# Performance work log

Hardware: AMD Instinct MI355X
Metric: run time of the kernel (lower is better)

The kernel has to match this reference:

```python
import jax, jax.numpy as jnp
import numpy as np

B, H, W = 32, 512, 384
V, F = 6890, 13776


def setup_inputs() -> dict:
    key = jax.random.key(0)
    ks = jax.random.split(key, 8)
    scale = jnp.array([W, H, 1.0], dtype=jnp.float32)
    verts_1 = jax.random.uniform(ks[0], (B, V, 3), dtype=jnp.float32) * scale
    verts_2 = jax.random.uniform(ks[1], (B, V, 3), dtype=jnp.float32) * scale
    # face index per pixel; -1 = background (uint32 0xFFFFFFFF sentinel in original)
    vis_1 = (jax.random.randint(ks[2], (B, H, W), 0, F + 1) - 1).astype(jnp.int32)
    vis_2 = (jax.random.randint(ks[3], (B, H, W), 0, F + 1) - 1).astype(jnp.int32)
    face = jax.random.randint(ks[4], (F, 3), 0, V).astype(jnp.int32)
    vis_sym_mask_1 = (jax.random.uniform(ks[5], (B, H, W)) < 0.5).astype(jnp.float32)
    sym = jax.random.randint(ks[6], (V,), 0, V)
    symmetric_table = jnp.concatenate([sym, jnp.array([-1])]).astype(jnp.int32)
    return {"verts_1": verts_1, "vis_1": vis_1, "verts_2": verts_2, "vis_2": vis_2,
            "face": face, "vis_sym_mask_1": vis_sym_mask_1, "symmetric_table": symmetric_table}


def _pix_grid(h, w):
    # (x, y) pixel coordinates, shape [h, w, 2]
    x = jnp.arange(w, dtype=jnp.float32)
    y = jnp.arange(h, dtype=jnp.float32)
    return jnp.stack(jnp.meshgrid(x, y, indexing="xy"), axis=-1)


def reference(verts_1, vis_1, verts_2, vis_2, face, vis_sym_mask_1, symmetric_table):
    v1 = verts_1[:, :, :2]  # [B,V,2]
    v2 = verts_2[:, :, :2]
    bg = vis_1 < 0
    fc = jnp.where(bg, 0, vis_1)  # safe face id per pixel

    # --- vis_2_onehot: which faces are visible in image 2 ---
    valid2 = vis_2 >= 0
    idx2 = jnp.where(valid2, vis_2, 0)
    bidx = jnp.arange(B)[:, None, None]
    vf2 = jnp.zeros((B, F), jnp.int32).at[bidx, idx2].add(valid2.astype(jnp.int32)) > 0

    # --- cal_corr: barycentric correspondence per pixel ---
    tri = face[fc]  # [B,H,W,3] vertex ids of the face under each pixel
    gather = jax.vmap(lambda verts, t: verts[t])  # per-batch fancy gather
    p1 = gather(v1, tri)  # [B,H,W,3,2] face verts in img1
    p = _pix_grid(H, W)  # [H,W,2]
    a, b_, c = p1[..., 0, :], p1[..., 1, :], p1[..., 2, :]
    e0, e1, e2 = b_ - a, c - a, p - a
    d00 = (e0 * e0).sum(-1); d01 = (e0 * e1).sum(-1); d11 = (e1 * e1).sum(-1)
    d20 = (e2 * e0).sum(-1); d21 = (e2 * e1).sum(-1)
    denom = d00 * d11 - d01 * d01
    denom = jnp.where(jnp.abs(denom) < 1e-12, 1.0, denom)
    wv = (d11 * d20 - d01 * d21) / denom
    ww = (d00 * d21 - d01 * d20) / denom
    bary = jnp.stack([1.0 - wv - ww, wv, ww], axis=-1)  # [B,H,W,3]

    vis2f = vf2[bidx, fc]  # face visible in img2?
    sym_tri = symmetric_table[tri]  # symmetric vertex ids (-1 = none)
    sym_ok = jnp.all(sym_tri >= 0, axis=-1) & (vis_sym_mask_1 > 0)
    use_sym = (~vis2f) & sym_ok & (~bg)
    tri2 = jnp.where(use_sym[..., None], jnp.where(sym_tri >= 0, sym_tri, 0), tri)
    p2 = gather(v2, tri2)  # [B,H,W,3,2] face verts in img2
    corr = jnp.einsum("bhwk,bhwkc->bhwc", bary, p2)  # [B,H,W,2] (u,v)

    has_corr = (~bg) & (vis2f | use_sym)
    corr_mask = jnp.where(bg, 2.0, jnp.where(has_corr, 0.0, 1.0)).astype(jnp.float32)
    corr = jnp.where(has_corr[..., None], corr, 0.0)

    # custom kernel outputs are detached in the original
    corr = jax.lax.stop_gradient(corr)
    corr_mask = jax.lax.stop_gradient(corr_mask)

    # --- pad to square ---
    pad = (H - W) // 2
    corr = corr + jnp.array([pad, 0], dtype=corr.dtype)
    corr = jnp.pad(corr, ((0, 0), (0, 0), (pad, pad), (0, 0)))
    corr_mask = jnp.pad(corr_mask[..., None], ((0, 0), (0, 0), (pad, pad), (0, 0)),
                        constant_values=2.0)  # [B,H,W+2p,1]
    Hp, Wp = H, W + 2 * pad

    # --- corr_to_flow (HWC) then fix_flow: grid = base + (corr - base), normalized ---
    base = _pix_grid(Hp, Wp)  # [Hp,Wp,2]
    flow = corr - base
    grid = base + flow
    gx = 2.0 * grid[..., 0] / max(Wp - 1, 1) - 1.0
    gy = 2.0 * grid[..., 1] / max(Hp - 1, 1) - 1.0
    out_grid = jnp.stack([gx, gy], axis=-1)  # [B,Hp,Wp,2]
    return out_grid, corr_mask
```

## Files before the change

kernel.cpp:

```cpp
#include <hip/hip_runtime.h>

#pragma clang fp contract(off)

#define B_ 32
#define H_ 512
#define W_ 384
#define V_ 6890
#define F_ 13776
#define PAD_ 64
#define WP_ 512


__global__ __launch_bounds__(256) void vf2_scatter_kernel(
    const int4* __restrict__ vis_2_v4, unsigned char* __restrict__ vf2)
{
    unsigned bid = blockIdx.x;
    unsigned cpx = gridDim.x >> 3;
    unsigned swz = (bid & 7u) * cpx + (bid >> 3);
    int idx = (int)(swz * blockDim.x + threadIdx.x);
    const int total4 = B_ * H_ * W_ / 4;
    if (idx >= total4) return;
    int4 v = vis_2_v4[idx];
    int b = idx / (H_ * W_ / 4);
    unsigned char* t = vf2 + (size_t)b * F_;
    if (v.x >= 0) t[v.x] = 1;
    if (v.y >= 0) t[v.y] = 1;
    if (v.z >= 0) t[v.z] = 1;
    if (v.w >= 0) t[v.w] = 1;
}

__global__ __launch_bounds__(256) void face_precompute_kernel(
    const float* __restrict__ verts_1,
    const float* __restrict__ verts_2,
    const int*   __restrict__ face,
    const int*   __restrict__ symtab,
    const unsigned char* __restrict__ vf2,
    float4* __restrict__ recs)
{
#pragma clang fp contract(off)
    int idx = blockIdx.x * blockDim.x + threadIdx.x;
    const int total = B_ * F_;
    if (idx >= total) return;
    int f = idx % F_;
    int b = idx / F_;

    int i0 = face[f * 3 + 0];
    int i1 = face[f * 3 + 1];
    int i2 = face[f * 3 + 2];

    const float* v1b = verts_1 + (size_t)b * (V_ * 3);
    float ax = v1b[i0 * 3 + 0], ay = v1b[i0 * 3 + 1];
    float bx = v1b[i1 * 3 + 0], by = v1b[i1 * 3 + 1];
    float cx = v1b[i2 * 3 + 0], cy = v1b[i2 * 3 + 1];

    float e0x = bx - ax, e0y = by - ay;
    float e1x = cx - ax, e1y = cy - ay;
    float d00 = (e0x * e0x) + (e0y * e0y);
    float d01 = (e0x * e1x) + (e0y * e1y);
    float d11 = (e1x * e1x) + (e1y * e1y);
    float denom = (d00 * d11) - (d01 * d01);
    if (fabsf(denom) < 1e-12f) denom = 1.0f;

    bool vis2f = vf2[idx] != 0;
    int s0 = symtab[i0], s1 = symtab[i1], s2 = symtab[i2];
    bool sym_ok = (s0 >= 0) && (s1 >= 0) && (s2 >= 0);

    int t0 = (!vis2f && sym_ok) ? s0 : i0;
    int t1 = (!vis2f && sym_ok) ? s1 : i1;
    int t2 = (!vis2f && sym_ok) ? s2 : i2;

    const float* v2b = verts_2 + (size_t)b * (V_ * 3);
    float q0x = v2b[t0 * 3 + 0], q0y = v2b[t0 * 3 + 1];
    float q1x = v2b[t1 * 3 + 0], q1y = v2b[t1 * 3 + 1];
    float q2x = v2b[t2 * 3 + 0], q2y = v2b[t2 * 3 + 1];

    double dd00 = (double)d00, dd01 = (double)d01, dd11 = (double)d11;
    double dden = (double)denom;
    double De0x = (double)e0x, De0y = (double)e0y;
    double De1x = (double)e1x, De1y = (double)e1y;

    double Ux = (dd11 * De0x - dd01 * De1x) / dden;
    double Uy = (dd11 * De0y - dd01 * De1y) / dden;
    double Vx = (dd00 * De1x - dd01 * De0x) / dden;
    double Vy = (dd00 * De1y - dd01 * De0y) / dden;

    double dq1x = (double)q1x - (double)q0x;
    double dq2x = (double)q2x - (double)q0x;
    double dq1y = (double)q1y - (double)q0y;
    double dq2y = (double)q2y - (double)q0y;

    double Bx = Ux * dq1x + Vx * dq2x;
    double Cx = Uy * dq1x + Vy * dq2x;
    double By = Ux * dq1y + Vx * dq2y;
    double Cy = Uy * dq1y + Vy * dq2y;

    double Apx = (double)q0x - (double)ax * Bx - (double)ay * Cx;
    double Apy = (double)q0y - (double)ax * By - (double)ay * Cy;

    unsigned flags = (vis2f ? 1u : 0u) | (sym_ok ? 2u : 0u);

    float4* r = recs + (size_t)idx * 2;
    r[0] = make_float4((float)Apx, (float)Bx, (float)Cx, (float)Apy);
    r[1] = make_float4((float)By, (float)Cy, __uint_as_float(flags), 0.0f);
}

__global__ __launch_bounds__(256) void flow_main_kernel(
    const int*   __restrict__ vis_1,
    const float* __restrict__ vis_sym_mask_1,
    const float4* __restrict__ recs,
    float* __restrict__ out_grid,
    float* __restrict__ corr_mask)
{
#pragma clang fp contract(off)
    unsigned bid = blockIdx.x;
    unsigned cpx = gridDim.x >> 3;
    unsigned swz = (bid & 7u) * cpx + (bid >> 3);
    int tid  = (int)(swz * blockDim.x + threadIdx.x);
    int base = tid * 4;
    const int total = B_ * H_ * WP_;
    if (base >= total) return;

    int xp  = base % WP_;
    int rem = base / WP_;
    int y   = rem % H_;
    int b   = rem / H_;

    float4* og4 = reinterpret_cast<float4*>(out_grid);
    float4* cm4 = reinterpret_cast<float4*>(corr_mask);

    if (xp < PAD_ || xp >= W_ + PAD_) {
        og4[(base >> 1) + 0] = make_float4(-1.0f, -1.0f, -1.0f, -1.0f);
        og4[(base >> 1) + 1] = make_float4(-1.0f, -1.0f, -1.0f, -1.0f);
        cm4[base >> 2]       = make_float4(2.0f, 2.0f, 2.0f, 2.0f);
        return;
    }

    int x   = xp - PAD_;
    int pin = (b * H_ + y) * W_ + x;

    int4   vv = *reinterpret_cast<const int4*>(vis_1 + pin);
    float4 mm = *reinterpret_cast<const float4*>(vis_sym_mask_1 + pin);

    int   vis[4] = { vv.x, vv.y, vv.z, vv.w };
    float msk[4] = { mm.x, mm.y, mm.z, mm.w };

    float4 R0[4], R1[4];
    bool   bgs[4];
    #pragma unroll
    for (int k = 0; k < 4; ++k) {
        bgs[k] = vis[k] < 0;
        int fc = bgs[k] ? 0 : vis[k];
        const float4* r = recs + ((size_t)b * F_ + fc) * 2;
        R0[k] = r[0];
        R1[k] = r[1];
    }

    float gxo[4], gyo[4], cmo[4];
    #pragma unroll
    for (int k = 0; k < 4; ++k) {
        float Apx = R0[k].x, Bx = R0[k].y, Cx = R0[k].z, Apy = R0[k].w;
        float By  = R1[k].x, Cy = R1[k].y;
        unsigned flags = __float_as_uint(R1[k].z);
        bool vis2f  = (flags & 1u) != 0;
        bool sym_ok = (flags & 2u) != 0;

        float px = (float)(x + k), py = (float)y;

        float corr_x = ((px * Bx) + (py * Cx)) + Apx;
        float corr_y = ((px * By) + (py * Cy)) + Apy;

        bool bg = bgs[k];
        bool use_sym  = (!vis2f) && sym_ok && (msk[k] > 0.0f) && (!bg);
        bool has_corr = (!bg) && (vis2f || use_sym);
        if (!has_corr) { corr_x = 0.0f; corr_y = 0.0f; }

        corr_x = corr_x + (float)PAD_;

        float base_x = (float)(xp + k), base_y = py;
        float fx = corr_x - base_x;
        float fy = corr_y - base_y;
        float gxv = base_x + fx;
        float gyv = base_y + fy;

        gxo[k] = ((2.0f * gxv) / (float)(WP_ - 1)) - 1.0f;
        gyo[k] = ((2.0f * gyv) / (float)(H_  - 1)) - 1.0f;
        cmo[k] = bg ? 2.0f : (has_corr ? 0.0f : 1.0f);
    }

    og4[(base >> 1) + 0] = make_float4(gxo[0], gyo[0], gxo[1], gyo[1]);
    og4[(base >> 1) + 1] = make_float4(gxo[2], gyo[2], gxo[3], gyo[3]);
    cm4[base >> 2]       = make_float4(cmo[0], cmo[1], cmo[2], cmo[3]);
}

extern "C" void kernel_launch(void* const* d_in, const int* in_sizes, int n_in,
                              void* d_out, int out_size, void* d_ws, size_t ws_size,
                              hipStream_t stream)
{
    const float* verts_1 = (const float*)d_in[0];
    const int*   vis_1   = (const int*)d_in[1];
    const float* verts_2 = (const float*)d_in[2];
    const int*   vis_2   = (const int*)d_in[3];
    const int*   face    = (const int*)d_in[4];
    const float* vis_sym = (const float*)d_in[5];
    const int*   symtab  = (const int*)d_in[6];

    float* out_grid  = (float*)d_out;
    float* corr_mask = (float*)d_out + (size_t)B_ * H_ * WP_ * 2;

    unsigned char* vf2 = (unsigned char*)d_ws;
    size_t rec_off = ((size_t)B_ * F_ + 63) & ~(size_t)63;
    float4* recs = (float4*)((unsigned char*)d_ws + rec_off);

    hipMemsetAsync(vf2, 0, (size_t)B_ * F_, stream);

    {
        const int total4 = B_ * H_ * W_ / 4;
        const int block  = 256;
        const int grid   = total4 / block;
        vf2_scatter_kernel<<<grid, block, 0, stream>>>(
            (const int4*)vis_2, vf2);
    }
    {
        const int total = B_ * F_;
        const int block = 256;
        face_precompute_kernel<<<(total + block - 1) / block, block, 0, stream>>>(
            verts_1, verts_2, face, symtab, vf2, recs);
    }
    {
        const int total = B_ * H_ * WP_;
        const int block = 256;
        const int grid  = total / (block * 4);
        flow_main_kernel<<<grid, block, 0, stream>>>(
            vis_1, vis_sym, recs, out_grid, corr_mask);
    }
}
```

Baseline: 94.66 us.

## Map one wavefront per row in flow kernel with nontemporal loads/stores

The main flow kernel now assigns a 64-lane wavefront to each output row. Each lane handles 6 interior pixels strided by 64, which removes the idle padding threads and gives coalesced per-element accesses. Streaming inputs and outputs use nontemporal loads and stores so they do not pollute the cache, and the vis_2 scatter load is also made nontemporal. The trade-off is narrower per-lane accesses (scalar or float2 instead of float4) in exchange for more gathers in flight per thread.

Measured after the change: 122.3 us. +29.2%, slower.

```diff
diff --git a/kernel.cpp b/kernel.cpp
--- a/kernel.cpp
+++ b/kernel.cpp
@@ -10,9 +10,14 @@
 #define PAD_ 64
 #define WP_ 512
 
+typedef int   vint4   __attribute__((ext_vector_type(4)));
+typedef float vfloat4 __attribute__((ext_vector_type(4)));
+typedef float vfloat2 __attribute__((ext_vector_type(2)));
+
+
 
 __global__ __launch_bounds__(256) void vf2_scatter_kernel(
-    const int4* __restrict__ vis_2_v4, unsigned char* __restrict__ vf2)
+    const vint4* __restrict__ vis_2_v4, unsigned char* __restrict__ vf2)
 {
     unsigned bid = blockIdx.x;
     unsigned cpx = gridDim.x >> 3;
@@ -20,7 +25,7 @@
     int idx = (int)(swz * blockDim.x + threadIdx.x);
     const int total4 = B_ * H_ * W_ / 4;
     if (idx >= total4) return;
-    int4 v = vis_2_v4[idx];
+    vint4 v = __builtin_nontemporal_load(vis_2_v4 + idx);
     int b = idx / (H_ * W_ / 4);
     unsigned char* t = vf2 + (size_t)b * F_;
     if (v.x >= 0) t[v.x] = 1;
@@ -115,81 +120,80 @@
     unsigned bid = blockIdx.x;
     unsigned cpx = gridDim.x >> 3;
     unsigned swz = (bid & 7u) * cpx + (bid >> 3);
-    int tid  = (int)(swz * blockDim.x + threadIdx.x);
-    int base = tid * 4;
-    const int total = B_ * H_ * WP_;
-    if (base >= total) return;
-
-    int xp  = base % WP_;
-    int rem = base / WP_;
-    int y   = rem % H_;
-    int b   = rem / H_;
-
-    float4* og4 = reinterpret_cast<float4*>(out_grid);
-    float4* cm4 = reinterpret_cast<float4*>(corr_mask);
-
-    if (xp < PAD_ || xp >= W_ + PAD_) {
-        og4[(base >> 1) + 0] = make_float4(-1.0f, -1.0f, -1.0f, -1.0f);
-        og4[(base >> 1) + 1] = make_float4(-1.0f, -1.0f, -1.0f, -1.0f);
-        cm4[base >> 2]       = make_float4(2.0f, 2.0f, 2.0f, 2.0f);
-        return;
-    }
-
-    int x   = xp - PAD_;
-    int pin = (b * H_ + y) * W_ + x;
-
-    int4   vv = *reinterpret_cast<const int4*>(vis_1 + pin);
-    float4 mm = *reinterpret_cast<const float4*>(vis_sym_mask_1 + pin);
-
-    int   vis[4] = { vv.x, vv.y, vv.z, vv.w };
-    float msk[4] = { mm.x, mm.y, mm.z, mm.w };
-
-    float4 R0[4], R1[4];
-    bool   bgs[4];
+    int gtid = (int)(swz * blockDim.x + threadIdx.x);
+    int row  = gtid >> 6;
+    int lane = (int)(threadIdx.x & 63u);
+    int y = row % H_;
+    int b = row / H_;
+
+    const int*   visrow = vis_1          + (size_t)row * W_;
+    const float* mskrow = vis_sym_mask_1 + (size_t)row * W_;
+    vfloat2*     ogrow  = (vfloat2*)out_grid + (size_t)row * WP_;
+    float*       cmrow  = corr_mask      + (size_t)row * WP_;
+
+    {
+        vfloat2 pv = { -1.0f, -1.0f };
+        __builtin_nontemporal_store(pv, ogrow + lane);
+        __builtin_nontemporal_store(pv, ogrow + 448 + lane);
+        __builtin_nontemporal_store(2.0f, cmrow + lane);
+        __builtin_nontemporal_store(2.0f, cmrow + 448 + lane);
+    }
+
+    int   vis[6];
+    float msk[6];
     #pragma unroll
-    for (int k = 0; k < 4; ++k) {
-        bgs[k] = vis[k] < 0;
-        int fc = bgs[k] ? 0 : vis[k];
+    for (int j = 0; j < 6; ++j) {
+        vis[j] = __builtin_nontemporal_load(visrow + j * 64 + lane);
+        msk[j] = __builtin_nontemporal_load(mskrow + j * 64 + lane);
+    }
+
+    float4 R0[6], R1[6];
+    bool   bgs[6];
+    #pragma unroll
+    for (int j = 0; j < 6; ++j) {
+        bgs[j] = vis[j] < 0;
+        int fc = bgs[j] ? 0 : vis[j];
         const float4* r = recs + ((size_t)b * F_ + fc) * 2;
-        R0[k] = r[0];
-        R1[k] = r[1];
-    }
-
-    float gxo[4], gyo[4], cmo[4];
+        R0[j] = r[0];
+        R1[j] = r[1];
+    }
+
     #pragma unroll
-    for (int k = 0; k < 4; ++k) {
-        float Apx = R0[k].x, Bx = R0[k].y, Cx = R0[k].z, Apy = R0[k].w;
-        float By  = R1[k].x, Cy = R1[k].y;
-        unsigned flags = __float_as_uint(R1[k].z);
+    for (int j = 0; j < 6; ++j) {
+        float Apx = R0[j].x, Bx = R0[j].y, Cx = R0[j].z, Apy = R0[j].w;
+        float By  = R1[j].x, Cy = R1[j].y;
+        unsigned flags = __float_as_uint(R1[j].z);
         bool vis2f  = (flags & 1u) != 0;
         bool sym_ok = (flags & 2u) != 0;
 
-        float px = (float)(x + k), py = (float)y;
+        int   x  = j * 64 + lane;
+        int   xp = x + PAD_;
+        float px = (float)x, py = (float)y;
 
         float corr_x = ((px * Bx) + (py * Cx)) + Apx;
         float corr_y = ((px * By) + (py * Cy)) + Apy;
 
-        bool bg = bgs[k];
-        bool use_sym  = (!vis2f) && sym_ok && (msk[k] > 0.0f) && (!bg);
+        bool bg = bgs[j];
+        bool use_sym  = (!vis2f) && sym_ok && (msk[j] > 0.0f) && (!bg);
         bool has_corr = (!bg) && (vis2f || use_sym);
         if (!has_corr) { corr_x = 0.0f; corr_y = 0.0f; }
 
         corr_x = corr_x + (float)PAD_;
 
-        float base_x = (float)(xp + k), base_y = py;
+        float base_x = (float)xp, base_y = py;
         float fx = corr_x - base_x;
         float fy = corr_y - base_y;
         float gxv = base_x + fx;
         float gyv = base_y + fy;
 
-        gxo[k] = ((2.0f * gxv) / (float)(WP_ - 1)) - 1.0f;
-        gyo[k] = ((2.0f * gyv) / (float)(H_  - 1)) - 1.0f;
-        cmo[k] = bg ? 2.0f : (has_corr ? 0.0f : 1.0f);
-    }
-
-    og4[(base >> 1) + 0] = make_float4(gxo[0], gyo[0], gxo[1], gyo[1]);
-    og4[(base >> 1) + 1] = make_float4(gxo[2], gyo[2], gxo[3], gyo[3]);
-    cm4[base >> 2]       = make_float4(cmo[0], cmo[1], cmo[2], cmo[3]);
+        float gx = ((2.0f * gxv) / (float)(WP_ - 1)) - 1.0f;
+        float gy = ((2.0f * gyv) / (float)(H_  - 1)) - 1.0f;
+        float cm = bg ? 2.0f : (has_corr ? 0.0f : 1.0f);
+
+        vfloat2 ov = { gx, gy };
+        __builtin_nontemporal_store(ov, ogrow + xp);
+        __builtin_nontemporal_store(cm, cmrow + xp);
+    }
 }
 
 extern "C" void kernel_launch(void* const* d_in, const int* in_sizes, int n_in,
@@ -211,14 +215,14 @@
     size_t rec_off = ((size_t)B_ * F_ + 63) & ~(size_t)63;
     float4* recs = (float4*)((unsigned char*)d_ws + rec_off);
 
-    hipMemsetAsync(vf2, 0, (size_t)B_ * F_, stream);
+    (void)hipMemsetAsync(vf2, 0, (size_t)B_ * F_, stream);
 
     {
         const int total4 = B_ * H_ * W_ / 4;
         const int block  = 256;
         const int grid   = total4 / block;
         vf2_scatter_kernel<<<grid, block, 0, stream>>>(
-            (const int4*)vis_2, vf2);
+            (const vint4*)vis_2, vf2);
     }
     {
         const int total = B_ * F_;
@@ -227,9 +231,9 @@
             verts_1, verts_2, face, symtab, vf2, recs);
     }
     {
-        const int total = B_ * H_ * WP_;
+        const int rows  = B_ * H_;
         const int block = 256;
-        const int grid  = total / (block * 4);
+        const int grid  = rows / 4;
         flow_main_kernel<<<grid, block, 0, stream>>>(
             vis_1, vis_sym, recs, out_grid, corr_mask);
     }
```
